# Kernel tuning notes

Measured on AMD Instinct MI355X. Metric: run time of the kernel, lower is better.

Reference implementation:

```python
import jax, jax.numpy as jnp
import numpy as np

N_NODES = 4096
N_EDGES = 32768
PE_DIM = 16
HIDDEN = 128


def setup_inputs() -> dict:
    key = jax.random.key(0)
    k_nodes, k_send, k_recv, k_w = jax.random.split(key, 4)
    nodes = jax.random.normal(k_nodes, (N_NODES, 8), dtype=jnp.float32)
    senders = jax.random.randint(k_send, (N_EDGES,), 0, N_NODES)
    receivers = jax.random.randint(k_recv, (N_EDGES,), 0, N_NODES)
    W = jax.random.normal(k_w, (PE_DIM, HIDDEN), dtype=jnp.float32) / np.sqrt(PE_DIM).astype(np.float32)
    b = jnp.zeros((HIDDEN,), dtype=jnp.float32)
    return {"nodes": nodes, "senders": senders, "receivers": receivers, "W": W, "b": b}


def reference(nodes, senders, receivers, W, b):
    n = nodes.shape[0]
    pe_dim = W.shape[0]
    # out-degree per node (clamped at 1, as in the original)
    ones = jnp.ones(senders.shape[0], dtype=jnp.float32)
    degree = jnp.maximum(jax.ops.segment_sum(ones, senders, num_segments=n), 1.0)
    inv_deg_e = (1.0 / degree)[senders]  # [E], per-edge 1/deg(sender)

    prob = jnp.eye(n, dtype=jnp.float32)  # [n, n] landing probabilities
    diags = []
    for _ in range(pe_dim):
        # gather sender rows, normalize, scatter-add into receiver rows
        msg = prob[senders] * inv_deg_e[:, None]           # [E, n]
        prob = jax.ops.segment_sum(msg, receivers, num_segments=n)  # [n, n]
        diags.append(jnp.diagonal(prob))                    # return probability A^k_ii
    pe = jnp.stack(diags, axis=-1)  # [n, pe_dim]
    return pe @ W + b               # [n, hidden]
```

## Files before the change

kernel.cpp:

```cpp
#include <hip/hip_runtime.h>

#define NN 4096
#define NE 32768
#define PED 16
#define HID 128
#define CW 16
#define NCHUNK 64
#define THREADS 1024
#define PASSES 4

typedef _Float16 h_t;
typedef _Float16 h8 __attribute__((ext_vector_type(8)));
typedef unsigned long long u64;

__device__ __forceinline__ int xp(int p) {
  int g = ((p & 3) << 1) | ((p >> 2) & 1);
  return ((p >> 2) << 7) | (g << 4);
}

__global__ __launch_bounds__(1024)
void prep_all(const int* __restrict__ senders, const int* __restrict__ receivers,
              int* __restrict__ rowperm_g, int* __restrict__ chunk_off_g,
              int* __restrict__ chunk_len_g,
              int2* __restrict__ esrc, int2* __restrict__ edst) {
  __shared__ int ld_out[NN];
  __shared__ int ld_d[NN];
  __shared__ int sortpos_l[NN];
  __shared__ int rowperm_l[NN];
  __shared__ float dinv_l[NN];
  __shared__ int fillc_l[NN];
  __shared__ int hist[64];
  __shared__ int hbase[64];
  __shared__ int coff[NCHUNK + 1];
  __shared__ int clen[NCHUNK];
  int t = threadIdx.x;

  for (int i = t; i < NN; i += 1024) { ld_out[i] = 0; ld_d[i] = 0; fillc_l[i] = 0; }
  if (t < 64) hist[t] = 0;
  __syncthreads();
  for (int e = t; e < NE; e += 1024) {
    atomicAdd(&ld_out[senders[e]], 1);
    atomicAdd(&ld_d[receivers[e]], 1);
  }
  __syncthreads();
  for (int r = t; r < NN; r += 1024) {
    int od = ld_out[r]; if (od < 1) od = 1;
    dinv_l[r] = 1.0f / (float)od;
    int d = ld_d[r]; if (d > 63) d = 63;
    ld_d[r] = d;
    atomicAdd(&hist[d], 1);
  }
  __syncthreads();
  if (t == 0) { int acc = 0; for (int i = 0; i < 64; ++i) { hbase[i] = acc; acc += hist[i]; } }
  __syncthreads();
  for (int r = t; r < NN; r += 1024) {
    int pos = atomicAdd(&hbase[ld_d[r]], 1);
    rowperm_l[pos] = r;
    sortpos_l[r] = pos;
  }
  __syncthreads();
  if (t < NCHUNK) {
    int m = 0;
    for (int i = 0; i < 64; ++i) { int d = ld_d[rowperm_l[(t << 6) + i]]; if (d > m) m = d; }
    clen[t] = (m + 1) & ~1;
  }
  __syncthreads();
  if (t == 0) {
    int acc = 0;
    for (int c = 0; c < NCHUNK; ++c) { coff[c] = acc; acc += clen[c] << 6; }
    coff[NCHUNK] = acc;
  }
  __syncthreads();
  for (int i = t; i < NN; i += 1024) rowperm_g[i] = rowperm_l[i];
  if (t < NCHUNK) chunk_len_g[t] = clen[t];
  if (t <= NCHUNK) chunk_off_g[t] = coff[t];
  for (int e = t; e < NE; e += 1024) {
    int r = receivers[e], s = senders[e];
    int p = sortpos_l[r];
    int tslot = atomicAdd(&fillc_l[r], 1);
    int slot = coff[p >> 6] + (tslot << 6) + (p & 63);
    esrc[slot] = make_int2(xp(sortpos_l[s]), __float_as_int(dinv_l[s]));
  }
  __threadfence();
  __syncthreads();
  int total = coff[NCHUNK];
  for (int i = t; i < 2048; i += 1024) edst[total + i] = make_int2(0, 0);
  if (t < NCHUNK * 8) {
    int c = t >> 3;
    int trk = t & 7;
    int base = coff[c];
    int len = clen[c];
    int l0 = trk << 3;
    int d[8];
    u64 freeL[8];
    int dmax = 0;
#pragma unroll
    for (int j = 0; j < 8; ++j) {
      int dd = ld_d[rowperm_l[(c << 6) + l0 + j]];
      d[j] = dd;
      if (dd > dmax) dmax = dd;
    }
    if (len > 63) {
#pragma unroll
      for (int j = 0; j < 8; ++j) {
        for (int tt = 0; tt < d[j]; ++tt) edst[base + (tt << 6) + l0 + j] = esrc[base + (tt << 6) + l0 + j];
        for (int tt = d[j]; tt < len; ++tt) edst[base + (tt << 6) + l0 + j] = make_int2(((tt + j) & 7) << 4, 0);
      }
      return;
    }
    u64 full = (len == 0) ? 0 : ((1ull << len) - 1);
#pragma unroll
    for (int j = 0; j < 8; ++j) freeL[j] = full;
    u64 fC[8];
#pragma unroll
    for (int q = 0; q < 8; ++q) fC[q] = full;
    for (int tt = 0; tt < dmax; ++tt) {
      int2 cur[8];
#pragma unroll
      for (int j = 0; j < 8; ++j) cur[j] = esrc[base + (tt << 6) + l0 + j];
#pragma unroll
      for (int j = 0; j < 8; ++j) {
        if (tt < d[j]) {
          int2 e = cur[j];
          int cls = (e.x >> 4) & 7;
          u64 fc = 0;
#pragma unroll
          for (int q = 0; q < 8; ++q) fc = (q == cls) ? fC[q] : fc;
          u64 avail = freeL[j] & fc;
          u64 pool = avail ? avail : freeL[j];
          u64 pick = pool & (~pool + 1);
          int slab = __builtin_ctzll(pick);
          freeL[j] &= ~pick;
          if (avail) {
#pragma unroll
            for (int q = 0; q < 8; ++q) if (q == cls) fC[q] &= ~pick;
          }
          edst[base + (slab << 6) + l0 + j] = e;
        }
      }
    }
#pragma unroll
    for (int j = 0; j < 8; ++j) {
      u64 rem = freeL[j];
      while (rem) {
        u64 pick = rem & (~rem + 1);
        rem &= rem - 1;
        int slab = __builtin_ctzll(pick);
        int cls = 0;
#pragma unroll
        for (int q = 7; q >= 0; --q) if (fC[q] & pick) cls = q;
#pragma unroll
        for (int q = 0; q < 8; ++q) if (q == cls) fC[q] &= ~pick;
        edst[base + (slab << 6) + l0 + j] = make_int2(cls << 4, 0);
      }
    }
  }
}


#define MIXL(acc, srcv) \
  asm("v_fma_mix_f32 %0, %1, %2, %0 op_sel_hi:[1,0,0]" : "+v"(acc) : "v"(srcv), "v"(w))
#define MIXH(acc, srcv) \
  asm("v_fma_mix_f32 %0, %1, %2, %0 op_sel:[1,0,0] op_sel_hi:[1,0,0]" : "+v"(acc) : "v"(srcv), "v"(w))

#define MIX16(lo, hi) \
  MIXL(a[0], lo.x);  MIXH(a[1], lo.x);  \
  MIXL(a[2], lo.y);  MIXH(a[3], lo.y);  \
  MIXL(a[4], lo.z);  MIXH(a[5], lo.z);  \
  MIXL(a[6], lo.w);  MIXH(a[7], lo.w);  \
  MIXL(a[8], hi.x);  MIXH(a[9], hi.x);  \
  MIXL(a[10], hi.y); MIXH(a[11], hi.y); \
  MIXL(a[12], hi.z); MIXH(a[13], hi.z); \
  MIXL(a[14], hi.w); MIXH(a[15], hi.w)

__global__ __launch_bounds__(THREADS, 4)
void fused_kernel(const int2* __restrict__ ell,
                  const int* __restrict__ chunk_off,
                  const int* __restrict__ chunk_len,
                  const int* __restrict__ rowperm,
                  const float* __restrict__ W,
                  const float* __restrict__ bvec,
                  float* __restrict__ out) {
  __shared__ __align__(16) h_t X[NN * CW];
  __shared__ float pe_lds[CW * PED];
  char* Xb = (char*)X;
  int c0 = blockIdx.x * CW;
  int tid = threadIdx.x;
  int wave = tid >> 6, lane = tid & 63;

  int baseB[PASSES], lenB[PASSES], djB[PASSES], xbW[PASSES];
#pragma unroll
  for (int pass = 0; pass < PASSES; ++pass) {
    int chunk = (pass << 4) + ((pass & 1) ? (15 - wave) : wave);
    baseB[pass] = chunk_off[chunk];
    lenB[pass] = chunk_len[chunk];
    djB[pass] = rowperm[(chunk << 6) + lane] - c0;
    xbW[pass] = xp((chunk << 6) + lane);
  }

  for (int p = tid; p < NN; p += THREADS) {
    int dd = rowperm[p] - c0;
    h8 lo8, hi8;
#pragma unroll
    for (int j = 0; j < 8; ++j) {
      lo8[j] = (h_t)((dd == j) ? 1.0f : 0.0f);
      hi8[j] = (h_t)((dd == 8 + j) ? 1.0f : 0.0f);
    }
    int xb = xp(p);
    *reinterpret_cast<h8*>(Xb + xb) = lo8;
    *reinterpret_cast<h8*>(Xb + (xb ^ 16)) = hi8;
  }
  __syncthreads();

  for (int k = 0; k < PED; ++k) {
    h8 rlo[PASSES], rhi[PASSES];
#pragma unroll
    for (int pass = 0; pass < PASSES; ++pass) {
      int base = baseB[pass];
      int len = lenB[pass];
      float a[16];
#pragma unroll
      for (int j = 0; j < 16; ++j) a[j] = 0.f;
      const int2* ep = ell + base + lane;
      int2 e0 = ep[0];
      int2 e1 = ep[64];
      int2 e2 = ep[128];
      int2 e3 = ep[192];
      int4 lo0 = *reinterpret_cast<const int4*>(Xb + e0.x);
      int4 hi0 = *reinterpret_cast<const int4*>(Xb + (e0.x ^ 16));
      for (int t = 0; t < len; t += 2) {
        int2 e4 = ep[256], e5 = ep[320];
        ep += 128;
        int4 lo1 = *reinterpret_cast<const int4*>(Xb + e1.x);
        int4 hi1 = *reinterpret_cast<const int4*>(Xb + (e1.x ^ 16));
        float w = __int_as_float(e0.y);
        MIX16(lo0, hi0);
        int4 nlo = *reinterpret_cast<const int4*>(Xb + e2.x);
        int4 nhi = *reinterpret_cast<const int4*>(Xb + (e2.x ^ 16));
        w = __int_as_float(e1.y);
        MIX16(lo1, hi1);
        e0 = e2; e1 = e3; e2 = e4; e3 = e5;
        lo0 = nlo; hi0 = nhi;
      }
      h8 plo, phi;
#pragma unroll
      for (int j = 0; j < 8; ++j) { plo[j] = (h_t)a[j]; phi[j] = (h_t)a[8 + j]; }
      rlo[pass] = plo; rhi[pass] = phi;
      int dj = djB[pass];
      if (dj >= 0 && dj < CW) {
        float dv = a[0];
#pragma unroll
        for (int j = 1; j < 16; ++j) dv = (dj == j) ? a[j] : dv;
        pe_lds[dj * PED + k] = dv;
      }
    }
    if (k != PED - 1) {
      __syncthreads();
#pragma unroll
      for (int pass = 0; pass < PASSES; ++pass) {
        int xb = xbW[pass];
        *reinterpret_cast<h8*>(Xb + xb) = rlo[pass];
        *reinterpret_cast<h8*>(Xb + (xb ^ 16)) = rhi[pass];
      }
      __syncthreads();
    }
  }
  __syncthreads();

  {
    int h = tid & 127;
    int r0 = tid >> 7;
    float wcol[PED];
#pragma unroll
    for (int kk = 0; kk < PED; ++kk) wcol[kk] = W[kk * HID + h];
    float bb = bvec[h];
#pragma unroll
    for (int half = 0; half < 2; ++half) {
      int row = r0 + (half << 3);
      float acc = bb;
#pragma unroll
      for (int kk = 0; kk < PED; ++kk) acc = fmaf(pe_lds[row * PED + kk], wcol[kk], acc);
      out[(size_t)(c0 + row) * HID + h] = acc;
    }
  }
}

extern "C" void kernel_launch(void* const* d_in, const int* in_sizes, int n_in,
                              void* d_out, int out_size, void* d_ws, size_t ws_size,
                              hipStream_t stream) {
  const int* senders = (const int*)d_in[1];
  const int* receivers = (const int*)d_in[2];
  const float* W = (const float*)d_in[3];
  const float* bvec = (const float*)d_in[4];
  float* out = (float*)d_out;

  char* p = (char*)d_ws;
  int* rowperm = (int*)p;   p += (size_t)NN * 4;
  int* chunk_off = (int*)p; p += 128 * 4;
  int* chunk_len = (int*)p; p += 128 * 4;
  size_t ell_slots = (size_t)64 * NE + 2048;
  int2* ell = (int2*)p;     p += ell_slots * sizeof(int2);
  int2* ell2 = (int2*)p;

  prep_all<<<1, 1024, 0, stream>>>(senders, receivers, rowperm, chunk_off, chunk_len, ell, ell2);
  fused_kernel<<<NN / CW, THREADS, 0, stream>>>(ell2, chunk_off, chunk_len, rowperm, W, bvec, out);
}
```

Before: 239.3 us.

## Split single-block preprocessing into permutation kernel and per-chunk parallel ELL build

The monolithic single-block prep kernel is split in two. A single-block kernel now computes degrees, the degree-sorted permutation and the chunk offsets. A second kernel with one block per chunk (64 blocks) builds each chunk's ELL slab in shared memory and then copies it to global memory. This spreads the serial edge scatter and slot-assignment work across many CUs and removes the global scratch ELL round trip. In exchange, every block rescans all edges to find its own, and there is an extra kernel launch.

```diff
diff --git a/kernel.cpp b/kernel.cpp
--- a/kernel.cpp
+++ b/kernel.cpp
@@ -19,109 +19,102 @@
 }
 
 __global__ __launch_bounds__(1024)
-void prep_all(const int* __restrict__ senders, const int* __restrict__ receivers,
-              int* __restrict__ rowperm_g, int* __restrict__ chunk_off_g,
-              int* __restrict__ chunk_len_g,
-              int2* __restrict__ esrc, int2* __restrict__ edst) {
+void perm_all(const int* __restrict__ senders, const int* __restrict__ receivers,
+              float* __restrict__ dinv_g, int* __restrict__ sortpos_g,
+              int* __restrict__ rowperm_g,
+              int* __restrict__ chunk_off_g, int* __restrict__ chunk_len_g) {
   __shared__ int ld_out[NN];
-  __shared__ int ld_d[NN];
-  __shared__ int sortpos_l[NN];
-  __shared__ int rowperm_l[NN];
-  __shared__ float dinv_l[NN];
-  __shared__ int fillc_l[NN];
+  __shared__ int ld_in[NN];
+  __shared__ int rp[NN];
   __shared__ int hist[64];
   __shared__ int hbase[64];
-  __shared__ int coff[NCHUNK + 1];
   __shared__ int clen[NCHUNK];
   int t = threadIdx.x;
-
-  for (int i = t; i < NN; i += 1024) { ld_out[i] = 0; ld_d[i] = 0; fillc_l[i] = 0; }
+  for (int i = t; i < NN; i += 1024) { ld_out[i] = 0; ld_in[i] = 0; }
   if (t < 64) hist[t] = 0;
   __syncthreads();
   for (int e = t; e < NE; e += 1024) {
     atomicAdd(&ld_out[senders[e]], 1);
-    atomicAdd(&ld_d[receivers[e]], 1);
+    atomicAdd(&ld_in[receivers[e]], 1);
   }
   __syncthreads();
   for (int r = t; r < NN; r += 1024) {
     int od = ld_out[r]; if (od < 1) od = 1;
-    dinv_l[r] = 1.0f / (float)od;
-    int d = ld_d[r]; if (d > 63) d = 63;
-    ld_d[r] = d;
+    dinv_g[r] = 1.0f / (float)od;
+    int d = ld_in[r]; if (d > 63) d = 63;
+    ld_in[r] = d;
     atomicAdd(&hist[d], 1);
   }
   __syncthreads();
   if (t == 0) { int acc = 0; for (int i = 0; i < 64; ++i) { hbase[i] = acc; acc += hist[i]; } }
   __syncthreads();
   for (int r = t; r < NN; r += 1024) {
-    int pos = atomicAdd(&hbase[ld_d[r]], 1);
-    rowperm_l[pos] = r;
-    sortpos_l[r] = pos;
-  }
-  __syncthreads();
+    int pos = atomicAdd(&hbase[ld_in[r]], 1);
+    rp[pos] = r;
+    sortpos_g[r] = pos;
+  }
+  __syncthreads();
+  for (int i = t; i < NN; i += 1024) rowperm_g[i] = rp[i];
   if (t < NCHUNK) {
     int m = 0;
-    for (int i = 0; i < 64; ++i) { int d = ld_d[rowperm_l[(t << 6) + i]]; if (d > m) m = d; }
+    for (int i = 0; i < 64; ++i) { int d = ld_in[rp[(t << 6) + i]]; if (d > m) m = d; }
     clen[t] = (m + 1) & ~1;
+    chunk_len_g[t] = clen[t];
   }
   __syncthreads();
   if (t == 0) {
     int acc = 0;
-    for (int c = 0; c < NCHUNK; ++c) { coff[c] = acc; acc += clen[c] << 6; }
-    coff[NCHUNK] = acc;
-  }
-  __syncthreads();
-  for (int i = t; i < NN; i += 1024) rowperm_g[i] = rowperm_l[i];
-  if (t < NCHUNK) chunk_len_g[t] = clen[t];
-  if (t <= NCHUNK) chunk_off_g[t] = coff[t];
-  for (int e = t; e < NE; e += 1024) {
-    int r = receivers[e], s = senders[e];
-    int p = sortpos_l[r];
-    int tslot = atomicAdd(&fillc_l[r], 1);
-    int slot = coff[p >> 6] + (tslot << 6) + (p & 63);
-    esrc[slot] = make_int2(xp(sortpos_l[s]), __float_as_int(dinv_l[s]));
-  }
-  __threadfence();
-  __syncthreads();
-  int total = coff[NCHUNK];
-  for (int i = t; i < 2048; i += 1024) edst[total + i] = make_int2(0, 0);
-  if (t < NCHUNK * 8) {
-    int c = t >> 3;
-    int trk = t & 7;
-    int base = coff[c];
-    int len = clen[c];
-    int l0 = trk << 3;
+    for (int c = 0; c < NCHUNK; ++c) { chunk_off_g[c] = acc; acc += clen[c] << 6; }
+    chunk_off_g[NCHUNK] = acc;
+  }
+}
+
+__global__ void build_ell(const int* __restrict__ senders, const int* __restrict__ receivers,
+                          const int* __restrict__ sortpos, const float* __restrict__ dinv,
+                          const int* __restrict__ chunk_off, const int* __restrict__ chunk_len,
+                          int2* __restrict__ edst) {
+  __shared__ int2 ellA[64 * 64];
+  __shared__ int2 ellB[64 * 64];
+  __shared__ int fillc[64];
+  int c = blockIdx.x;
+  int tid = threadIdx.x;
+  int base = chunk_off[c];
+  int len = chunk_len[c];
+  if (tid < 64) fillc[tid] = 0;
+  __syncthreads();
+  for (int e = tid; e < NE; e += 512) {
+    int r = receivers[e];
+    int p = sortpos[r];
+    if ((p >> 6) == c) {
+      int s = senders[e];
+      int l = p & 63;
+      int ts = atomicAdd(&fillc[l], 1);
+      if (ts < 64) ellA[(ts << 6) + l] = make_int2(xp(sortpos[s]), __float_as_int(dinv[s]));
+    }
+  }
+  __syncthreads();
+  if (tid < 8) {
+    int l0 = tid << 3;
     int d[8];
     u64 freeL[8];
     int dmax = 0;
 #pragma unroll
     for (int j = 0; j < 8; ++j) {
-      int dd = ld_d[rowperm_l[(c << 6) + l0 + j]];
+      int dd = fillc[l0 + j]; if (dd > 63) dd = 63;
       d[j] = dd;
       if (dd > dmax) dmax = dd;
     }
-    if (len > 63) {
-#pragma unroll
-      for (int j = 0; j < 8; ++j) {
-        for (int tt = 0; tt < d[j]; ++tt) edst[base + (tt << 6) + l0 + j] = esrc[base + (tt << 6) + l0 + j];
-        for (int tt = d[j]; tt < len; ++tt) edst[base + (tt << 6) + l0 + j] = make_int2(((tt + j) & 7) << 4, 0);
-      }
-      return;
-    }
-    u64 full = (len == 0) ? 0 : ((1ull << len) - 1);
+    u64 full = (len >= 64) ? ~0ull : ((len == 0) ? 0 : ((1ull << len) - 1));
+    u64 fC[8];
 #pragma unroll
     for (int j = 0; j < 8; ++j) freeL[j] = full;
-    u64 fC[8];
 #pragma unroll
     for (int q = 0; q < 8; ++q) fC[q] = full;
     for (int tt = 0; tt < dmax; ++tt) {
-      int2 cur[8];
-#pragma unroll
-      for (int j = 0; j < 8; ++j) cur[j] = esrc[base + (tt << 6) + l0 + j];
 #pragma unroll
       for (int j = 0; j < 8; ++j) {
         if (tt < d[j]) {
-          int2 e = cur[j];
+          int2 e = ellA[(tt << 6) + l0 + j];
           int cls = (e.x >> 4) & 7;
           u64 fc = 0;
 #pragma unroll
@@ -135,7 +128,7 @@
 #pragma unroll
             for (int q = 0; q < 8; ++q) if (q == cls) fC[q] &= ~pick;
           }
-          edst[base + (slab << 6) + l0 + j] = e;
+          ellB[(slab << 6) + l0 + j] = e;
         }
       }
     }
@@ -151,9 +144,16 @@
         for (int q = 7; q >= 0; --q) if (fC[q] & pick) cls = q;
 #pragma unroll
         for (int q = 0; q < 8; ++q) if (q == cls) fC[q] &= ~pick;
-        edst[base + (slab << 6) + l0 + j] = make_int2(cls << 4, 0);
-      }
-    }
+        ellB[(slab << 6) + l0 + j] = make_int2(cls << 4, 0);
+      }
+    }
+  }
+  __syncthreads();
+  int n = len << 6;
+  for (int i = tid; i < n; i += 512) edst[base + i] = ellB[i];
+  if (c == 0) {
+    int total = chunk_off[NCHUNK];
+    for (int i = tid; i < 2048; i += 512) edst[total + i] = make_int2(0, 0);
   }
 }
 
@@ -296,12 +296,15 @@
 
   char* p = (char*)d_ws;
   int* rowperm = (int*)p;   p += (size_t)NN * 4;
+  int* sortpos = (int*)p;   p += (size_t)NN * 4;
+  float* dinv = (float*)p;  p += (size_t)NN * 4;
   int* chunk_off = (int*)p; p += 128 * 4;
   int* chunk_len = (int*)p; p += 128 * 4;
-  size_t ell_slots = (size_t)64 * NE + 2048;
-  int2* ell = (int2*)p;     p += ell_slots * sizeof(int2);
   int2* ell2 = (int2*)p;
 
-  prep_all<<<1, 1024, 0, stream>>>(senders, receivers, rowperm, chunk_off, chunk_len, ell, ell2);
+  perm_all<<<1, 1024, 0, stream>>>(senders, receivers, dinv, sortpos, rowperm,
+                                   chunk_off, chunk_len);
+  build_ell<<<NCHUNK, 512, 0, stream>>>(senders, receivers, sortpos, dinv,
+                                        chunk_off, chunk_len, ell2);
   fused_kernel<<<NN / CW, THREADS, 0, stream>>>(ell2, chunk_off, chunk_len, rowperm, W, bvec, out);
 }
```

Result: faster. 227.3 us (-5.0%).
